# Kernel optimization log

Measured on AMD Instinct MI355X. Metric: run time of the kernel, lower is better.

## Reference

```python
import jax, jax.numpy as jnp
import numpy as np

N = 50000            # nodes
E = 800000           # random edges (self loops added in reference, per PyG default)
D_IN, D1, D2, D_OUT = 256, 128, 64, 40
SLOPE = 0.2          # GATv2Conv default negative_slope


def _glorot(key, shape):
    fan_in, fan_out = shape[0], shape[-1]
    s = jnp.sqrt(6.0 / (fan_in + fan_out))
    return jax.random.uniform(key, shape, jnp.float32, -s, s)


def setup_inputs() -> dict:
    key = jax.random.key(0)
    ks = jax.random.split(key, 16)
    inp = {
        "x": jax.random.normal(ks[0], (N, D_IN), jnp.float32),
        "edge_index": jax.random.randint(ks[1], (2, E), 0, N),
    }
    dims = [(D_IN, D1), (D1, D2), (D2, D_OUT)]
    k = 2
    for i, (di, do) in enumerate(dims, 1):
        inp[f"W{i}l"] = _glorot(ks[k], (di, do)); k += 1
        inp[f"W{i}r"] = _glorot(ks[k], (di, do)); k += 1
        inp[f"b{i}l"] = jnp.zeros((do,), jnp.float32)
        inp[f"b{i}r"] = jnp.zeros((do,), jnp.float32)
        inp[f"a{i}"]  = _glorot(ks[k], (do,));    k += 1
        inp[f"c{i}"]  = jnp.zeros((do,), jnp.float32)
    return inp


def _gatv2(x, src, dst, Wl, bl, Wr, br, att, bias):
    # GATv2Conv, heads=1: lin_l on source nodes, lin_r on target nodes
    xl = x @ Wl + bl                     # [N, do] source transform
    xr = x @ Wr + br                     # [N, do] target transform
    e = jax.nn.leaky_relu(xl[src] + xr[dst], SLOPE)   # [Etot, do]
    logits = e @ att                     # [Etot]
    # segment softmax over incoming edges of each dst node
    m = jax.ops.segment_max(logits, dst, num_segments=N)
    ex = jnp.exp(logits - m[dst])
    denom = jax.ops.segment_sum(ex, dst, num_segments=N)
    alpha = ex / denom[dst]              # [Etot]
    out = jax.ops.segment_sum(alpha[:, None] * xl[src], dst, num_segments=N)
    return out + bias


def reference(x, edge_index,
              W1l, W1r, b1l, b1r, a1, c1,
              W2l, W2r, b2l, b2r, a2, c2,
              W3l, W3r, b3l, b3r, a3, c3):
    loop = jnp.arange(N, dtype=edge_index.dtype)
    src = jnp.concatenate([edge_index[0], loop])   # add_self_loops=True
    dst = jnp.concatenate([edge_index[1], loop])
    h = jax.nn.relu(_gatv2(x, src, dst, W1l, b1l, W1r, b1r, a1, c1))
    h = jax.nn.relu(_gatv2(h, src, dst, W2l, b2l, W2r, b2r, a2, c2))
    h = _gatv2(h, src, dst, W3l, b3l, W3r, b3r, a3, c3)
    return jax.nn.log_softmax(h, axis=1)
```

## Files before the change

### kernel.cpp

```cpp
#include <hip/hip_runtime.h>
#include <math.h>

#define NN 50000
#define NE 800000
#define SLOPE 0.2f
#define NEGX (-1e30f)
#define CH 8192

typedef _Float16 h8 __attribute__((ext_vector_type(8)));
typedef _Float16 h2 __attribute__((ext_vector_type(2)));
typedef float f8 __attribute__((ext_vector_type(8)));
typedef float v4f __attribute__((ext_vector_type(4)));

__device__ __forceinline__ h8 hzero(){ h8 z = {0,0,0,0,0,0,0,0}; return z; }
__device__ __forceinline__ f8 fzero(){ f8 z = {0,0,0,0,0,0,0,0}; return z; }

__device__ __forceinline__ void pack_one(const float* __restrict__ W,
                                         _Float16* __restrict__ Wp,
                                         int DO, int K, int NT, int t){
  int KC = K >> 5;
  if (t >= NT * KC * 64) return;
  int lane = t & 63;
  int rest = t >> 6;
  int c  = rest % KC;
  int nt = rest / KC;
  int col = nt * 16 + (lane & 15);
  int k0  = c * 32 + ((lane >> 4) << 3);
  _Float16 o[8];
#pragma unroll
  for (int j = 0; j < 8; j++){
    float v = (col < DO) ? W[(k0 + j) * DO + col] : 0.f;
    o[j] = (_Float16)v;
  }
  *(ulonglong2*)(Wp + (size_t)t * 8) = *(ulonglong2*)o;
}

__global__ __launch_bounds__(256) void k_pack_hist(
    const float* W1l, const float* W1r, const float* W2l,
    const float* W2r, const float* W3l, const float* W3r,
    _Float16* p1l, _Float16* p1r, _Float16* p2l,
    _Float16* p2r, _Float16* p3l, _Float16* p3r,
    const int* __restrict__ ei, int* __restrict__ gbp){
  __shared__ int h[256];
  int b = blockIdx.x, t = threadIdx.x;
  if (b < 44){
    if      (b < 16) pack_one(W1l, p1l, 128, 256, 8, (b     ) * 256 + t);
    else if (b < 32) pack_one(W1r, p1r, 128, 256, 8, (b - 16) * 256 + t);
    else if (b < 36) pack_one(W2l, p2l,  64, 128, 4, (b - 32) * 256 + t);
    else if (b < 40) pack_one(W2r, p2r,  64, 128, 4, (b - 36) * 256 + t);
    else if (b < 42) pack_one(W3l, p3l,  40,  64, 3, (b - 40) * 256 + t);
    else             pack_one(W3r, p3r,  40,  64, 3, (b - 42) * 256 + t);
  } else {
    int hb = b - 44;
    h[t] = 0;
    __syncthreads();
    int e0 = hb * 12500;
    for (int i = t; i < 12500; i += 256)
      atomicAdd(&h[ei[NE + e0 + i] >> 8], 1);
    __syncthreads();
    gbp[hb * 256 + t] = h[t];
  }
}

__global__ __launch_bounds__(256) void k_scan(const int* __restrict__ gbp,
                                              int* __restrict__ base,
                                              int* __restrict__ bcur,
                                              int* __restrict__ row_ptr,
                                              int* __restrict__ dcnt){
  __shared__ int s[256];
  int t = threadIdx.x;
  dcnt[t] = 0;
  int v = 0;
#pragma unroll 8
  for (int i = 0; i < 64; i++) v += gbp[i * 256 + t];
  s[t] = v; __syncthreads();
  for (int off = 1; off < 256; off <<= 1){
    int a = (t >= off) ? s[t - off] : 0;
    __syncthreads(); s[t] += a; __syncthreads();
  }
  int ex = s[t] - v;
  base[t] = ex;
  bcur[t] = ex;
  if (t == 255){ base[256] = s[255]; row_ptr[NN] = s[255]; }
}

__global__ __launch_bounds__(256) void k_bscatter(const int* __restrict__ ei,
                                                  int* __restrict__ bcur,
                                                  unsigned* __restrict__ pk_out){
  __shared__ unsigned pk[CH];
  __shared__ int h[256];
  int t = threadIdx.x;
  int e0 = blockIdx.x * CH;
  h[t] = 0;
  __syncthreads();
  int n = NE - e0; if (n > CH) n = CH;
  for (int i = t; i < n; i += 256){
    int e = e0 + i;
    int s = ei[e], d = ei[NE + e];
    pk[i] = (unsigned)s | ((unsigned)(d & 255) << 16) | ((unsigned)(d >> 8) << 24);
    atomicAdd(&h[d >> 8], 1);
  }
  __syncthreads();
  int c = h[t];
  if (c) h[t] = atomicAdd(&bcur[t], c);
  __syncthreads();
  for (int i = t; i < n; i += 256){
    unsigned u = pk[i];
    int pos = atomicAdd(&h[u >> 24], 1);
    pk_out[pos] = u;
  }
}

__global__ __launch_bounds__(256) void k_bcsr(const unsigned* __restrict__ pk,
                                              const int* __restrict__ base,
                                              int* __restrict__ row_ptr,
                                              int* __restrict__ csr_src,
                                              int* __restrict__ dcnt){
  __shared__ int h[256], s[256];
  int t = threadIdx.x;
  int b = blockIdx.x;
  int lo = base[b], hi = base[b + 1];
  h[t] = 0;
  __syncthreads();
  for (int i = lo + t; i < hi; i += 256)
    atomicAdd(&h[(pk[i] >> 16) & 255], 1);
  __syncthreads();
  int v = h[t];
  s[t] = v; __syncthreads();
  for (int off = 1; off < 256; off <<= 1){
    int a = (t >= off) ? s[t - off] : 0;
    __syncthreads(); s[t] += a; __syncthreads();
  }
  int ex = lo + s[t] - v;
  int node = b * 256 + t;
  if (node < NN) row_ptr[node] = ex;
  h[t] = ex;
  s[t] = 0;
  __syncthreads();
  if (node < NN) atomicAdd(&s[v < 255 ? v : 255], 1);
  __syncthreads();
  if (s[t]) atomicAdd(&dcnt[t], s[t]);
  for (int i = lo + t; i < hi; i += 256){
    unsigned u = pk[i];
    int pos = atomicAdd(&h[(u >> 16) & 255], 1);
    csr_src[pos] = (int)(u & 0xFFFFu);
  }
}

__global__ __launch_bounds__(256) void k_dscan(const int* __restrict__ dcnt,
                                               int* __restrict__ dcur){
  __shared__ int s[256];
  int t = threadIdx.x;
  int v = dcnt[t];
  s[t] = v; __syncthreads();
  for (int off = 1; off < 256; off <<= 1){
    int a = (t >= off) ? s[t - off] : 0;
    __syncthreads(); s[t] += a; __syncthreads();
  }
  dcur[t] = s[t] - v;
}

__global__ __launch_bounds__(256) void k_dscatter(const int* __restrict__ row_ptr,
                                                  int* __restrict__ dcur,
                                                  int* __restrict__ perm){
  __shared__ int lh[256];
  int t = threadIdx.x;
  int node = blockIdx.x * 256 + t;
  lh[t] = 0;
  __syncthreads();
  int bin = -1;
  if (node < NN){
    int deg = row_ptr[node + 1] - row_ptr[node];
    bin = deg < 255 ? deg : 255;
    atomicAdd(&lh[bin], 1);
  }
  __syncthreads();
  int c = lh[t];
  int bp = c ? atomicAdd(&dcur[t], c) : 0;
  __syncthreads();
  lh[t] = bp;
  __syncthreads();
  if (node < NN){
    int pos = atomicAdd(&lh[bin], 1);
    perm[pos] = node;
  }
}

template<typename TI, int K, int DO>
__global__ __launch_bounds__(256, 4) void gemm_direct(
    const TI* __restrict__ X,
    const _Float16* __restrict__ Wpl, const float* __restrict__ bl,
    const _Float16* __restrict__ Wpr, const float* __restrict__ br,
    _Float16* __restrict__ Yl, _Float16* __restrict__ Yr)
{
  constexpr int KC = K / 32;
  constexpr int NT = (DO + 15) / 16;
  int lane = threadIdx.x & 63;
  int wv   = threadIdx.x >> 6;
  int row0 = (blockIdx.x * 4 + wv) * 16;
  int arow = lane & 15;
  int koff = lane >> 4;
  int lrow = row0 + arow;
  int crow = (lrow < NN) ? lrow : 0;

  h8 afrag[KC];
  if constexpr (sizeof(TI) == 4){
    const float* Xr = (const float*)X + (size_t)crow * K + koff * 8;
#pragma unroll
    for (int c = 0; c < KC; c++){
      float4 v0 = *reinterpret_cast<const float4*>(Xr + c * 32);
      float4 v1 = *reinterpret_cast<const float4*>(Xr + c * 32 + 4);
      h8 a;
      a[0]=(_Float16)v0.x; a[1]=(_Float16)v0.y; a[2]=(_Float16)v0.z; a[3]=(_Float16)v0.w;
      a[4]=(_Float16)v1.x; a[5]=(_Float16)v1.y; a[6]=(_Float16)v1.z; a[7]=(_Float16)v1.w;
      afrag[c] = a;
    }
  } else {
    const _Float16* Xr = (const _Float16*)X + (size_t)crow * K + koff * 8;
#pragma unroll
    for (int c = 0; c < KC; c++)
      afrag[c] = *reinterpret_cast<const h8*>(Xr + c * 32);
  }

#pragma unroll
  for (int side = 0; side < 2; side++){
    const _Float16* Wp = side ? Wpr : Wpl;
    const float* bias = side ? br : bl;
    _Float16* Y = side ? Yr : Yl;
#pragma unroll
    for (int nt = 0; nt < NT; nt++){
      v4f acc = {0.f, 0.f, 0.f, 0.f};
#pragma unroll
      for (int c = 0; c < KC; c++){
        h8 b = *reinterpret_cast<const h8*>(Wp + (size_t)((nt * KC + c) * 64 + lane) * 8);
        acc = __builtin_amdgcn_mfma_f32_16x16x32_f16(afrag[c], b, acc, 0, 0, 0);
      }
      int col = nt * 16 + arow;
      if (col < DO){
        float bv = bias[col];
        int rbase = row0 + koff * 4;
#pragma unroll
        for (int r = 0; r < 4; r++){
          int orow = rbase + r;
          if (orow < NN) Y[(size_t)orow * DO + col] = (_Float16)(acc[r] + bv);
        }
      }
    }
  }
}

__device__ __forceinline__ float edge_logit(h8 x, h8 xrv, h8 attv){
  h8 t = x + xrv;
  h8 l = __builtin_elementwise_max(t, t * (_Float16)SLOPE);
  const h2* lp = (const h2*)&l;
  const h2* ap = (const h2*)&attv;
  h2 d = lp[0] * ap[0];
  d += lp[1] * ap[1];
  d += lp[2] * ap[2];
  d += lp[3] * ap[3];
  return (float)d[0] + (float)d[1];
}

template<int LPG>
__device__ __forceinline__ float gsum(float v){
#pragma unroll
  for (int off = 1; off < LPG; off <<= 1) v += __shfl_xor(v, off, 64);
  return v;
}
template<int LPG>
__device__ __forceinline__ void gsum2(float& a, float& b){
#pragma unroll
  for (int off = 1; off < LPG; off <<= 1){
    a += __shfl_xor(a, off, 64);
    b += __shfl_xor(b, off, 64);
  }
}
template<int LPG>
__device__ __forceinline__ float gmax(float v){
#pragma unroll
  for (int off = 1; off < LPG; off <<= 1) v = fmaxf(v, __shfl_xor(v, off, 64));
  return v;
}

template<int DO, int LPG, int DO2>
__global__ __launch_bounds__(256) void agg_gemm(
    const _Float16* __restrict__ xl, const _Float16* __restrict__ xr,
    const int* __restrict__ csr_src, const int* __restrict__ row_ptr,
    const int* __restrict__ perm,
    const float* __restrict__ att, const float* __restrict__ bias,
    const _Float16* __restrict__ Wpl2, const float* __restrict__ bl2,
    const _Float16* __restrict__ Wpr2, const float* __restrict__ br2,
    _Float16* __restrict__ Yl, _Float16* __restrict__ Yr)
{
  constexpr int G = 64 / LPG;
  constexpr int NPB = 4 * G;
  constexpr int LK = DO + 8;
  constexpr int KC2 = DO / 32;
  constexpr int NT2 = (DO2 + 15) / 16;
  constexpr int MT = NPB / 16;
  __shared__ _Float16 hs[NPB * LK];
  __shared__ int nodeOf[NPB];

  int tid  = threadIdx.x;
  int lane = tid & 63;
  int wid  = tid >> 6;

  unsigned seg = (unsigned)(blockIdx.x * 1021u) % gridDim.x;
  if (tid < NPB){
    int idx = seg * NPB + tid;
    nodeOf[tid] = (idx < NN) ? perm[idx] : NN;
  }
  __syncthreads();

  int g = lane / LPG, p = lane % LPG;
  int nodeLocal = wid * G + g;
  int node = nodeOf[nodeLocal];
  int cbase = p * 8;
  bool nvalid = node < NN;
  int nodeC = nvalid ? node : 0;

  h8 attv, xrv, xlv;
  {
    float4 a0 = *reinterpret_cast<const float4*>(att + cbase);
    float4 a1 = *reinterpret_cast<const float4*>(att + cbase + 4);
    attv[0]=(_Float16)a0.x; attv[1]=(_Float16)a0.y; attv[2]=(_Float16)a0.z; attv[3]=(_Float16)a0.w;
    attv[4]=(_Float16)a1.x; attv[5]=(_Float16)a1.y; attv[6]=(_Float16)a1.z; attv[7]=(_Float16)a1.w;
    xrv = *reinterpret_cast<const h8*>(xr + nodeC * DO + cbase);
    xlv = *reinterpret_cast<const h8*>(xl + nodeC * DO + cbase);
  }
  float s = gsum<LPG>(edge_logit(xlv, xrv, attv));
  float wS = __expf(s);
  float denA = wS, denB = 0.f;
  f8 accA, accB;
  {
    f8 xf = __builtin_convertvector(xlv, f8);
    accA = xf * wS;
    accB = fzero();
  }

  int e0 = row_ptr[nodeC];
  int e1 = nvalid ? row_ptr[nodeC + 1] : e0;
  int e = e0;
  for (; e + 1 < e1; e += 2){
    int sA = csr_src[e], sB = csr_src[e + 1];
    h8 xA = *reinterpret_cast<const h8*>(xl + sA * DO + cbase);
    h8 xB = *reinterpret_cast<const h8*>(xl + sB * DO + cbase);
    float pA = edge_logit(xA, xrv, attv);
    float pB = edge_logit(xB, xrv, attv);
    gsum2<LPG>(pA, pB);
    float wA = __expf(pA), wB = __expf(pB);
    denA += wA; denB += wB;
    accA = __builtin_convertvector(xA, f8) * wA + accA;
    accB = __builtin_convertvector(xB, f8) * wB + accB;
  }
  if (e < e1){
    int sA = csr_src[e];
    h8 xA = *reinterpret_cast<const h8*>(xl + sA * DO + cbase);
    float pA = gsum<LPG>(edge_logit(xA, xrv, attv));
    float w = __expf(pA);
    denA += w;
    accA = __builtin_convertvector(xA, f8) * w + accA;
  }

  {
    float inv = 1.0f / (denA + denB);
    f8 sum = (accA + accB) * inv;
    float4 b0 = *reinterpret_cast<const float4*>(bias + cbase);
    float4 b1 = *reinterpret_cast<const float4*>(bias + cbase + 4);
    f8 bv = {b0.x, b0.y, b0.z, b0.w, b1.x, b1.y, b1.z, b1.w};
    sum += bv;
    sum = __builtin_elementwise_max(sum, fzero());
    *reinterpret_cast<h8*>(&hs[nodeLocal * LK + cbase]) = __builtin_convertvector(sum, h8);
  }
  __syncthreads();

  int arow = lane & 15;
  int koff = lane >> 4;
  int mt = (MT == 1) ? 0 : (wid >> 1);
  h8 afrag[KC2];
#pragma unroll
  for (int c = 0; c < KC2; c++)
    afrag[c] = *reinterpret_cast<const h8*>(&hs[(mt * 16 + arow) * LK + koff * 8 + c * 32]);

  int side = wid & 1;
  const _Float16* Wp = side ? Wpr2 : Wpl2;
  const float* bias2 = side ? br2 : bl2;
  _Float16* Y = side ? Yr : Yl;
  int nt_begin = (MT == 1) ? (wid >> 1) * (NT2 / 2) : 0;
  int nt_end   = (MT == 1) ? nt_begin + NT2 / 2 : NT2;
  for (int nt = nt_begin; nt < nt_end; nt++){
    v4f acc = {0.f, 0.f, 0.f, 0.f};
#pragma unroll
    for (int c = 0; c < KC2; c++){
      h8 b = *reinterpret_cast<const h8*>(Wp + (size_t)((nt * KC2 + c) * 64 + lane) * 8);
      acc = __builtin_amdgcn_mfma_f32_16x16x32_f16(afrag[c], b, acc, 0, 0, 0);
    }
    int col = nt * 16 + arow;
    if (col < DO2){
      float bv = bias2[col];
      int lrbase = mt * 16 + koff * 4;
#pragma unroll
      for (int r = 0; r < 4; r++){
        int orow = nodeOf[lrbase + r];
        if (orow < NN) Y[(size_t)orow * DO2 + col] = (_Float16)(acc[r] + bv);
      }
    }
  }
}

template<int DO, int LPG>
__global__ __launch_bounds__(256) void gat_agg_out(
    const _Float16* __restrict__ xl, const _Float16* __restrict__ xr,
    const int* __restrict__ csr_src, const int* __restrict__ row_ptr,
    const int* __restrict__ perm,
    const float* __restrict__ att, const float* __restrict__ bias,
    float* __restrict__ out)
{
  constexpr int G = 64 / LPG;
  constexpr int NPB = 4 * G;
  __shared__ int nodeOf[NPB];
  int tid  = threadIdx.x;
  int lane = tid & 63;
  int wid  = tid >> 6;

  unsigned seg = (unsigned)(blockIdx.x * 1021u) % gridDim.x;
  if (tid < NPB){
    int idx = seg * NPB + tid;
    nodeOf[tid] = (idx < NN) ? perm[idx] : NN;
  }
  __syncthreads();

  int g = lane / LPG;
  int p = lane % LPG;
  int node = nodeOf[wid * G + g];
  bool nvalid = node < NN;
  int nodeC = nvalid ? node : 0;
  int cbase = p * 8;
  bool ok = (cbase < DO);

  h8 attv = hzero(), xrv = hzero(), xlv = hzero();
  if (ok){
    float4 a0 = *reinterpret_cast<const float4*>(att + cbase);
    float4 a1 = *reinterpret_cast<const float4*>(att + cbase + 4);
    attv[0]=(_Float16)a0.x; attv[1]=(_Float16)a0.y; attv[2]=(_Float16)a0.z; attv[3]=(_Float16)a0.w;
    attv[4]=(_Float16)a1.x; attv[5]=(_Float16)a1.y; attv[6]=(_Float16)a1.z; attv[7]=(_Float16)a1.w;
    xrv = *reinterpret_cast<const h8*>(xr + nodeC * DO + cbase);
    xlv = *reinterpret_cast<const h8*>(xl + nodeC * DO + cbase);
  }

  float s = gsum<LPG>(edge_logit(xlv, xrv, attv));
  float wS = __expf(s);
  float denA = wS, denB = 0.f;
  f8 accA, accB;
  {
    f8 xf = __builtin_convertvector(xlv, f8);
    accA = xf * wS;
    accB = fzero();
  }

  int e0 = row_ptr[nodeC];
  int e1 = nvalid ? row_ptr[nodeC + 1] : e0;
  int e = e0;
  for (; e + 1 < e1; e += 2){
    int sA = csr_src[e], sB = csr_src[e + 1];
    h8 xA = ok ? *reinterpret_cast<const h8*>(xl + sA * DO + cbase) : hzero();
    h8 xB = ok ? *reinterpret_cast<const h8*>(xl + sB * DO + cbase) : hzero();
    float pA = edge_logit(xA, xrv, attv);
    float pB = edge_logit(xB, xrv, attv);
    gsum2<LPG>(pA, pB);
    float wA = __expf(pA), wB = __expf(pB);
    denA += wA; denB += wB;
    accA = __builtin_convertvector(xA, f8) * wA + accA;
    accB = __builtin_convertvector(xB, f8) * wB + accB;
  }
  if (e < e1){
    int sA = csr_src[e];
    h8 xA = ok ? *reinterpret_cast<const h8*>(xl + sA * DO + cbase) : hzero();
    float pA = gsum<LPG>(edge_logit(xA, xrv, attv));
    float w = __expf(pA);
    denA += w;
    accA = __builtin_convertvector(xA, f8) * w + accA;
  }

  float inv = 1.0f / (denA + denB);
  f8 sumv = (accA + accB) * inv;
  float v[8]; float lmax = NEGX;
#pragma unroll
  for (int j = 0; j < 8; j++){
    v[j] = ok ? (sumv[j] + bias[cbase + j]) : NEGX;
    lmax = fmaxf(lmax, v[j]);
  }
  lmax = gmax<LPG>(lmax);
  float lsum = 0.f;
#pragma unroll
  for (int j = 0; j < 8; j++) lsum += __expf(v[j] - lmax);
  lsum = gsum<LPG>(lsum);
  if (ok && nvalid){
    float lg = lmax + __logf(lsum);
    float* op = (float*)out + node * DO + cbase;
    float4 o0, o1;
    o0.x = v[0] - lg; o0.y = v[1] - lg; o0.z = v[2] - lg; o0.w = v[3] - lg;
    o1.x = v[4] - lg; o1.y = v[5] - lg; o1.z = v[6] - lg; o1.w = v[7] - lg;
    *reinterpret_cast<float4*>(op) = o0;
    *reinterpret_cast<float4*>(op + 4) = o1;
  }
}

extern "C" void kernel_launch(void* const* d_in, const int* in_sizes, int n_in,
                              void* d_out, int out_size, void* d_ws, size_t ws_size,
                              hipStream_t stream) {
  const float* x   = (const float*)d_in[0];
  const int*   ei  = (const int*)d_in[1];
  const float* W1l = (const float*)d_in[2];  const float* W1r = (const float*)d_in[3];
  const float* b1l = (const float*)d_in[4];  const float* b1r = (const float*)d_in[5];
  const float* a1  = (const float*)d_in[6];  const float* c1  = (const float*)d_in[7];
  const float* W2l = (const float*)d_in[8];  const float* W2r = (const float*)d_in[9];
  const float* b2l = (const float*)d_in[10]; const float* b2r = (const float*)d_in[11];
  const float* a2  = (const float*)d_in[12]; const float* c2  = (const float*)d_in[13];
  const float* W3l = (const float*)d_in[14]; const float* W3r = (const float*)d_in[15];
  const float* b3l = (const float*)d_in[16]; const float* b3r = (const float*)d_in[17];
  const float* a3  = (const float*)d_in[18]; const float* c3  = (const float*)d_in[19];
  float* outp = (float*)d_out;

  _Float16* xl1 = (_Float16*)d_ws;
  _Float16* xr1 = xl1 + 6400000;
  _Float16* xl2 = xr1 + 6400000;
  _Float16* xr2 = xl2 + 3200000;
  _Float16* xl3 = xr2 + 3200000;
  _Float16* xr3 = xl3 + 2000000;
  _Float16* wp1l = xr3 + 2000000;
  _Float16* wp1r = wp1l + 32768;
  _Float16* wp2l = wp1r + 32768;
  _Float16* wp2r = wp2l + 8192;
  _Float16* wp3l = wp2r + 8192;
  _Float16* wp3r = wp3l + 3072;
  unsigned* pk   = (unsigned*)(wp3r + 3072);
  int* csr_src   = (int*)(pk + NE);
  int* row_ptr   = csr_src + NE;
  int* gbp       = row_ptr + 50001;
  int* base      = gbp + 16384;
  int* bcur      = base + 257;
  int* perm      = bcur + 256;
  int* dcnt      = perm + NN;
  int* dcur      = dcnt + 256;

  const int GB = (NN + 63) / 64;
  const int SB = (NE + CH - 1) / CH;
  const int FB1 = (NN + 15) / 16;
  const int FB2 = (NN + 31) / 32;
  const int AB3 = (NN + 31) / 32;

  k_pack_hist<<<108, 256, 0, stream>>>(W1l, W1r, W2l, W2r, W3l, W3r,
                                       wp1l, wp1r, wp2l, wp2r, wp3l, wp3r,
                                       ei, gbp);
  k_scan<<<1, 256, 0, stream>>>(gbp, base, bcur, row_ptr, dcnt);
  k_bscatter<<<SB, 256, 0, stream>>>(ei, bcur, pk);
  k_bcsr<<<196, 256, 0, stream>>>(pk, base, row_ptr, csr_src, dcnt);
  k_dscan<<<1, 256, 0, stream>>>(dcnt, dcur);
  k_dscatter<<<196, 256, 0, stream>>>(row_ptr, dcur, perm);

  gemm_direct<float,256,128><<<GB, 256, 0, stream>>>(x, wp1l, b1l, wp1r, b1r, xl1, xr1);

  agg_gemm<128,16,64><<<FB1, 256, 0, stream>>>(xl1, xr1, csr_src, row_ptr, perm,
                                               a1, c1, wp2l, b2l, wp2r, b2r, xl2, xr2);

  agg_gemm<64,8,40><<<FB2, 256, 0, stream>>>(xl2, xr2, csr_src, row_ptr, perm,
                                             a2, c2, wp3l, b3l, wp3r, b3r, xl3, xr3);

  gat_agg_out<40,8><<<AB3, 256, 0, stream>>>(xl3, xr3, csr_src, row_ptr, perm, a3, c3, outp);
}
```

Before: 291.5 us.

## Fold degree scan into dscatter, use DPP reductions and fdot2 logits

Removes the separate single-block k_dscan launch: each k_dscatter block now recomputes the 256-bin degree prefix scan locally, and dcur is zeroed in k_scan and used as a relative offset. Group reductions (sum/max) switch from __shfl_xor to DPP row moves, and the edge logit dot product uses fdot2 with fp32 accumulation instead of packed half multiplies. The goal is to cut one launch and shuffle latency in the aggregation kernels. In exchange every dscatter block repeats the redundant scan, and the DPP control codes must match the lane group sizes.

Result: faster. 285.4 us (-2.1%).

```diff
diff --git a/kernel.cpp b/kernel.cpp
--- a/kernel.cpp
+++ b/kernel.cpp
@@ -66,10 +66,12 @@
                                               int* __restrict__ base,
                                               int* __restrict__ bcur,
                                               int* __restrict__ row_ptr,
-                                              int* __restrict__ dcnt){
+                                              int* __restrict__ dcnt,
+                                              int* __restrict__ dcur){
   __shared__ int s[256];
   int t = threadIdx.x;
   dcnt[t] = 0;
+  dcur[t] = 0;
   int v = 0;
 #pragma unroll 8
   for (int i = 0; i < 64; i++) v += gbp[i * 256 + t];
@@ -147,26 +149,15 @@
   }
 }
 
-__global__ __launch_bounds__(256) void k_dscan(const int* __restrict__ dcnt,
-                                               int* __restrict__ dcur){
-  __shared__ int s[256];
-  int t = threadIdx.x;
-  int v = dcnt[t];
-  s[t] = v; __syncthreads();
-  for (int off = 1; off < 256; off <<= 1){
-    int a = (t >= off) ? s[t - off] : 0;
-    __syncthreads(); s[t] += a; __syncthreads();
-  }
-  dcur[t] = s[t] - v;
-}
-
 __global__ __launch_bounds__(256) void k_dscatter(const int* __restrict__ row_ptr,
+                                                  const int* __restrict__ dcnt,
                                                   int* __restrict__ dcur,
                                                   int* __restrict__ perm){
-  __shared__ int lh[256];
+  __shared__ int lh[256], sc[256];
   int t = threadIdx.x;
   int node = blockIdx.x * 256 + t;
   lh[t] = 0;
+  int dv = dcnt[t];
   __syncthreads();
   int bin = -1;
   if (node < NN){
@@ -174,9 +165,15 @@
     bin = deg < 255 ? deg : 255;
     atomicAdd(&lh[bin], 1);
   }
-  __syncthreads();
+  sc[t] = dv;
+  __syncthreads();
+  for (int off = 1; off < 256; off <<= 1){
+    int a = (t >= off) ? sc[t - off] : 0;
+    __syncthreads(); sc[t] += a; __syncthreads();
+  }
+  int gbase = sc[t] - dv;
   int c = lh[t];
-  int bp = c ? atomicAdd(&dcur[t], c) : 0;
+  int bp = c ? (gbase + atomicAdd(&dcur[t], c)) : 0;
   __syncthreads();
   lh[t] = bp;
   __syncthreads();
@@ -249,37 +246,44 @@
   }
 }
 
+template<int CTRL>
+__device__ __forceinline__ float dppmv(float v){
+  int x = __builtin_amdgcn_update_dpp(0, __float_as_int(v), CTRL, 0xF, 0xF, true);
+  return __int_as_float(x);
+}
+
+template<int LPG>
+__device__ __forceinline__ float gsum(float v){
+  v += dppmv<177>(v);
+  v += dppmv<78>(v);
+  if (LPG >= 8)  v += dppmv<0x141>(v);
+  if (LPG == 16) v += dppmv<0x140>(v);
+  return v;
+}
+template<int LPG>
+__device__ __forceinline__ void gsum2(float& a, float& b){
+  a = gsum<LPG>(a);
+  b = gsum<LPG>(b);
+}
+template<int LPG>
+__device__ __forceinline__ float gmax(float v){
+  v = fmaxf(v, dppmv<177>(v));
+  v = fmaxf(v, dppmv<78>(v));
+  if (LPG >= 8)  v = fmaxf(v, dppmv<0x141>(v));
+  if (LPG == 16) v = fmaxf(v, dppmv<0x140>(v));
+  return v;
+}
+
 __device__ __forceinline__ float edge_logit(h8 x, h8 xrv, h8 attv){
   h8 t = x + xrv;
   h8 l = __builtin_elementwise_max(t, t * (_Float16)SLOPE);
   const h2* lp = (const h2*)&l;
   const h2* ap = (const h2*)&attv;
-  h2 d = lp[0] * ap[0];
-  d += lp[1] * ap[1];
-  d += lp[2] * ap[2];
-  d += lp[3] * ap[3];
-  return (float)d[0] + (float)d[1];
-}
-
-template<int LPG>
-__device__ __forceinline__ float gsum(float v){
-#pragma unroll
-  for (int off = 1; off < LPG; off <<= 1) v += __shfl_xor(v, off, 64);
-  return v;
-}
-template<int LPG>
-__device__ __forceinline__ void gsum2(float& a, float& b){
-#pragma unroll
-  for (int off = 1; off < LPG; off <<= 1){
-    a += __shfl_xor(a, off, 64);
-    b += __shfl_xor(b, off, 64);
-  }
-}
-template<int LPG>
-__device__ __forceinline__ float gmax(float v){
-#pragma unroll
-  for (int off = 1; off < LPG; off <<= 1) v = fmaxf(v, __shfl_xor(v, off, 64));
-  return v;
+  float d = __builtin_amdgcn_fdot2(lp[0], ap[0], 0.f, false);
+  d = __builtin_amdgcn_fdot2(lp[1], ap[1], d, false);
+  d = __builtin_amdgcn_fdot2(lp[2], ap[2], d, false);
+  d = __builtin_amdgcn_fdot2(lp[3], ap[3], d, false);
+  return d;
 }
 
 template<int DO, int LPG, int DO2>
@@ -553,11 +557,10 @@
   k_pack_hist<<<108, 256, 0, stream>>>(W1l, W1r, W2l, W2r, W3l, W3r,
                                        wp1l, wp1r, wp2l, wp2r, wp3l, wp3r,
                                        ei, gbp);
-  k_scan<<<1, 256, 0, stream>>>(gbp, base, bcur, row_ptr, dcnt);
+  k_scan<<<1, 256, 0, stream>>>(gbp, base, bcur, row_ptr, dcnt, dcur);
   k_bscatter<<<SB, 256, 0, stream>>>(ei, bcur, pk);
   k_bcsr<<<196, 256, 0, stream>>>(pk, base, row_ptr, csr_src, dcnt);
-  k_dscan<<<1, 256, 0, stream>>>(dcnt, dcur);
-  k_dscatter<<<196, 256, 0, stream>>>(row_ptr, dcur, perm);
+  k_dscatter<<<196, 256, 0, stream>>>(row_ptr, dcnt, dcur, perm);
 
   gemm_direct<float,256,128><<<GB, 256, 0, stream>>>(x, wp1l, b1l, wp1r, b1r, xl1, xr1);
 
```
